# Kernel tuning notes

Hardware: AMD Instinct MI355X
Metric: run time of the kernel (lower is better)

Reference implementation:

```python
import jax, jax.numpy as jnp
import numpy as np

_EPS = 1e-8
_ALPHA = 160.0  # bilateral spatial sigma
_BETA = 3.0     # bilateral color sigma
_GAMMA = 3.0    # spatial-filter sigma
_NUM_ITERS = 5
_L = 21
_H = 96
_W = 96


def _spatial_features(h, w, sigma):
    # [h, w, 2] grid of (x, y)/sigma, matching torch _spatial_features
    x = jnp.arange(w, dtype=jnp.float32) / sigma
    y = jnp.arange(h, dtype=jnp.float32) / sigma
    xx = jnp.broadcast_to(x[None, :], (h, w))
    yy = jnp.broadcast_to(y[:, None], (h, w))
    return jnp.stack([xx, yy], axis=2)


def _gauss_kernel(f):
    # f: [N, d] -> exact Gaussian kernel exp(-0.5 ||f_i - f_j||^2), [N, N]
    sq = jnp.sum(f * f, axis=1)
    d2 = sq[:, None] + sq[None, :] - 2.0 * (f @ f.T)
    return jnp.exp(-0.5 * jnp.maximum(d2, 0.0))


def setup_inputs() -> dict:
    key = jax.random.key(0)
    k1, k2 = jax.random.split(key)
    image = jax.random.uniform(k1, (1, 3, _H, _W), dtype=jnp.float32)
    logits = jax.random.normal(k2, (1, _L, _H, _W), dtype=jnp.float32)
    eye = jnp.eye(_L, dtype=jnp.float32)
    return {
        "image": image,
        "logits": logits,
        "spatial_ker_weights": 3.0 * eye,
        "bilateral_ker_weights": 5.0 * eye,
        "compatibility_matrix": eye,
    }


def reference(image, logits, spatial_ker_weights, bilateral_ker_weights, compatibility_matrix):
    img = image[0]        # [3, h, w]
    unary = logits[0]     # [L, h, w]
    L, h, w = unary.shape
    N = h * w

    # Filter kernels (exact Gaussian filtering that the permutohedral lattice approximates)
    xy_s = _spatial_features(h, w, _GAMMA).reshape(N, 2)
    xy_b = _spatial_features(h, w, _ALPHA)
    rgb = (img / _BETA).transpose(1, 2, 0)  # [h, w, 3]
    feat_b = jnp.concatenate([xy_b, rgb], axis=2).reshape(N, 5)

    K_s = _gauss_kernel(xy_s)    # [N, N]
    K_b = _gauss_kernel(feat_b)  # [N, N]
    norm_s = 1.0 / (jnp.sum(K_s, axis=1) + _EPS)  # [N]
    norm_b = 1.0 / (jnp.sum(K_b, axis=1) + _EPS)

    unary_flat = unary.reshape(L, N)
    cur = unary_flat
    for _ in range(_NUM_ITERS):
        q = jax.nn.softmax(cur, axis=0)           # softmax over labels, [L, N]
        sp = spatial_ker_weights @ ((q @ K_s) * norm_s)    # K symmetric
        bl = bilateral_ker_weights @ ((q @ K_b) * norm_b)
        cur = compatibility_matrix @ (sp + bl) + unary_flat
    return cur.reshape(1, L, h, w)
```

## Files before the change

### kernel.cpp

```cpp
#include <hip/hip_runtime.h>

#define NPIX 9216
#define NL   21
#define WW   96
#define RAD  16
#define JS   16
#define NJC  576
#define NST  9
#define NIB  72
#define NBIL (NIB * JS)
#define NSPT 756
#define L2E  1.44269504088896340736f

typedef __bf16 bf16x8 __attribute__((ext_vector_type(8)));
typedef float  f32x16 __attribute__((ext_vector_type(16)));

__device__ __forceinline__ float fexp2(float x) { return __builtin_amdgcn_exp2f(x); }
__device__ __forceinline__ unsigned pkbf(float lo, float hi) {
    unsigned r;
    asm("v_cvt_pk_bf16_f32 %0, %1, %2" : "=v"(r) : "v"(lo), "v"(hi));
    return r;
}

__global__ __launch_bounds__(256) void featK(const float* __restrict__ img,
                                             __bf16* __restrict__ FiT8, __bf16* __restrict__ Fj8,
                                             float* __restrict__ norm_s, __bf16* __restrict__ QhT) {
    int i = blockIdx.x * 256 + threadIdx.x;
    if (i >= NPIX) return;
    int y = i / WW, x = i - y * WW;
    float f0 = (float)x * (1.0f / 160.0f);
    float f1 = (float)y * (1.0f / 160.0f);
    float f2 = img[0 * NPIX + i] * (1.0f / 3.0f);
    float f3 = img[1 * NPIX + i] * (1.0f / 3.0f);
    float f4 = img[2 * NPIX + i] * (1.0f / 3.0f);
    float st = 0.5f * (f0*f0 + f1*f1 + f2*f2 + f3*f3 + f4*f4) * L2E;
    __bf16* a = Fj8 + (size_t)i * 16;
    __bf16* b = FiT8 + (size_t)i * 16;
    a[0]=(__bf16)(f0*L2E); a[1]=(__bf16)(f1*L2E); a[2]=(__bf16)(f2*L2E);
    a[3]=(__bf16)(f3*L2E); a[4]=(__bf16)(f4*L2E); a[5]=(__bf16)st; a[6]=(__bf16)1.0f;
    b[0]=(__bf16)f0; b[1]=(__bf16)f1; b[2]=(__bf16)f2; b[3]=(__bf16)f3; b[4]=(__bf16)f4;
    b[5]=(__bf16)-1.0f; b[6]=(__bf16)(-st);
    #pragma unroll
    for (int k = 7; k < 16; k++) { a[k] = (__bf16)0.0f; b[k] = (__bf16)0.0f; }
    QhT[(size_t)21 * NPIX + i] = (__bf16)1.0f;
    #pragma unroll
    for (int l = 22; l < 32; l++) QhT[(size_t)l * NPIX + i] = (__bf16)0.0f;
    const float cs = (-0.5f / 9.0f) * L2E;
    float sx = 0.f, sy = 0.f;
    int xa = max(0, x - RAD), xb = min(WW - 1, x + RAD);
    int ya = max(0, y - RAD), yb = min(WW - 1, y + RAD);
    for (int t = xa; t <= xb; t++) { float dx = (float)(x - t); sx += fexp2(cs * dx * dx); }
    for (int t = ya; t <= yb; t++) { float dy = (float)(y - t); sy += fexp2(cs * dy * dy); }
    norm_s[i] = 1.0f / (sx * sy + 1e-8f);
}

__global__ __launch_bounds__(448) void matK(const float* __restrict__ Cm, const float* __restrict__ Wsm,
                                            const float* __restrict__ Wbm,
                                            float* __restrict__ Ms, float* __restrict__ Mb) {
    int t = threadIdx.x;
    if (t >= NL * NL) return;
    int l = t / NL, p = t - l * NL;
    float a = 0.f, b = 0.f;
    for (int m = 0; m < NL; m++) {
        float c = Cm[l * NL + m];
        a = fmaf(c, Wsm[m * NL + p], a);
        b = fmaf(c, Wbm[m * NL + p], b);
    }
    Ms[t] = a; Mb[t] = b;
}

__global__ __launch_bounds__(256) void smax0(const float* __restrict__ cur, __bf16* __restrict__ QhT) {
    int i = blockIdx.x * 256 + threadIdx.x;
    if (i >= NPIX) return;
    float v[NL]; float m = -1e30f;
    #pragma unroll
    for (int l = 0; l < NL; l++) { v[l] = cur[l * NPIX + i]; m = fmaxf(m, v[l]); }
    float s = 0.f;
    #pragma unroll
    for (int l = 0; l < NL; l++) { v[l] = fexp2((v[l] - m) * L2E); s += v[l]; }
    float inv = 1.0f / s;
    #pragma unroll
    for (int l = 0; l < NL; l++) QhT[(size_t)l * NPIX + i] = (__bf16)(v[l] * inv);
}

__global__ __launch_bounds__(256) void spatX(const __bf16* __restrict__ QhT, float* __restrict__ S1) {
    __shared__ float wt[33];
    int t = threadIdx.x;
    if (t < 33) { float d = (float)(t - RAD); wt[t] = fexp2((-0.5f / 9.0f) * L2E * d * d); }
    __syncthreads();
    int tid = blockIdx.x * 256 + t;
    int l = tid / NPIX, rem = tid - l * NPIX;
    int y = rem / WW, x1 = rem - y * WW;
    const __bf16* row = QhT + (size_t)l * NPIX + y * WW;
    float acc = 0.f;
    #pragma unroll
    for (int d = 0; d < 33; d++) {
        int x2 = x1 - RAD + d;
        if ((unsigned)x2 < WW) acc = fmaf(wt[d], (float)row[x2], acc);
    }
    S1[tid] = acc;
}

__global__ __launch_bounds__(256) void fusedYB(const __bf16* __restrict__ QhT,
                                               const __bf16* __restrict__ FiT8,
                                               const __bf16* __restrict__ Fj8,
                                               float* __restrict__ part,
                                               const float* __restrict__ S1,
                                               const float* __restrict__ norm_s,
                                               float* __restrict__ Sp) {
    __shared__ __bf16 sQ[2][32][72];
    __shared__ __bf16 sFj[2][64][24];
    __shared__ float wt[33];
    int t = threadIdx.x;

    if (blockIdx.x >= NBIL) {
        if (t < 33) { float d = (float)(t - RAD); wt[t] = fexp2((-0.5f / 9.0f) * L2E * d * d); }
        __syncthreads();
        int tid = (blockIdx.x - NBIL) * 256 + t;
        int l = tid / NPIX, rem = tid - l * NPIX;
        int y1 = rem / WW, x = rem - y1 * WW;
        const float* col = S1 + l * NPIX + x;
        float acc = 0.f;
        #pragma unroll
        for (int d = 0; d < 33; d++) {
            int y2 = y1 - RAD + d;
            if ((unsigned)y2 < WW) acc = fmaf(wt[d], col[y2 * WW], acc);
        }
        Sp[tid] = acc * norm_s[rem];
        return;
    }

    int lane = t & 63;
    int w = t >> 6;
    int n = lane & 31, kb = lane >> 5;
    int jc = blockIdx.x / NIB;
    int ib = blockIdx.x - jc * NIB;
    int ibase = ib * 128 + w * 32;

    bf16x8 b1 = *reinterpret_cast<const bf16x8*>(FiT8 + (size_t)(ibase + n) * 16 + kb * 8);

    int qr = t >> 3, qc = t & 7;
    int fr = t >> 1, fh = t & 1;
    int jbeg = jc * NJC;
    const __bf16* qsrc = QhT + (size_t)qr * NPIX + jbeg;
    const __bf16* fsrc = Fj8 + (size_t)jbeg * 16;

    float4 gq = *reinterpret_cast<const float4*>(qsrc + qc * 8);
    float4 gf;
    if (t < 128) gf = *reinterpret_cast<const float4*>(fsrc + fr * 16 + fh * 8);
    *reinterpret_cast<float4*>(&sQ[0][qr][qc * 8]) = gq;
    if (t < 128) *reinterpret_cast<float4*>(&sFj[0][fr][fh * 8]) = gf;

    f32x16 acc = {};
    const f32x16 z = {};
    int cur = 0;
    for (int s = 0; s < NST; s++) {
        __syncthreads();
        bool pf = (s + 1 < NST);
        if (pf) {
            int jo = (s + 1) * 64;
            gq = *reinterpret_cast<const float4*>(qsrc + jo + qc * 8);
            if (t < 128) gf = *reinterpret_cast<const float4*>(fsrc + (size_t)(jo + fr) * 16 + fh * 8);
        }
        #pragma unroll
        for (int t2 = 0; t2 < 2; t2++) {
            int t32 = t2 * 32;
            bf16x8 a1 = *reinterpret_cast<const bf16x8*>(&sFj[cur][t32 + n][kb * 8]);
            f32x16 d = __builtin_amdgcn_mfma_f32_32x32x16_bf16(a1, b1, z, 0, 0, 0);
            float e[16];
            #pragma unroll
            for (int q = 0; q < 16; q++) e[q] = fexp2(d[q]);
            #pragma unroll
            for (int h = 0; h < 2; h++) {
                unsigned w0 = pkbf(e[8*h+0], e[8*h+1]);
                unsigned w1 = pkbf(e[8*h+2], e[8*h+3]);
                unsigned w2 = pkbf(e[8*h+4], e[8*h+5]);
                unsigned w3 = pkbf(e[8*h+6], e[8*h+7]);
                asm volatile("v_permlane32_swap_b32 %0, %1" : "+v"(w0), "+v"(w2));
                asm volatile("v_permlane32_swap_b32 %0, %1" : "+v"(w1), "+v"(w3));
                union { int4 u4; bf16x8 h8; } bb;
                bb.u4 = make_int4(w0, w1, w2, w3);
                bf16x8 qa = *reinterpret_cast<const bf16x8*>(&sQ[cur][n][t32 + h * 16 + kb * 8]);
                acc = __builtin_amdgcn_mfma_f32_32x32x16_bf16(qa, bb.h8, acc, 0, 0, 0);
            }
        }
        if (pf) {
            int nx = cur ^ 1;
            *reinterpret_cast<float4*>(&sQ[nx][qr][qc * 8]) = gq;
            if (t < 128) *reinterpret_cast<float4*>(&sFj[nx][fr][fh * 8]) = gf;
        }
        cur ^= 1;
    }
    float* p = part + (size_t)jc * 22 * NPIX + ibase + n;
    #pragma unroll
    for (int q = 0; q < 16; q++) {
        int l = (q & 3) + 8 * (q >> 2) + 4 * kb;
        if (l < 22) p[(size_t)l * NPIX] = acc[q];
    }
}

__global__ __launch_bounds__(256) void combZ(const float* __restrict__ Sp, const float* __restrict__ part,
                                             const float* __restrict__ Ms, const float* __restrict__ Mb,
                                             const float* __restrict__ unary, float* __restrict__ outp,
                                             __bf16* __restrict__ QhT, int wq) {
    __shared__ float sMs[NL * NL], sMb[NL * NL];
    int t = threadIdx.x;
    for (int k = t; k < NL * NL; k += 256) { sMs[k] = Ms[k]; sMb[k] = Mb[k]; }
    __syncthreads();
    int i = blockIdx.x * 256 + t;
    if (i >= NPIX) return;
    float bl[22];
    #pragma unroll
    for (int l = 0; l < 22; l++) bl[l] = 0.0f;
    for (int jc = 0; jc < JS; jc++) {
        const float* p = part + (size_t)jc * 22 * NPIX + i;
        #pragma unroll
        for (int l = 0; l < 22; l++) bl[l] += p[(size_t)l * NPIX];
    }
    float inv = 1.0f / (bl[21] + 1e-8f);
    float sp[NL], v[NL];
    #pragma unroll
    for (int p = 0; p < NL; p++) { sp[p] = Sp[p * NPIX + i]; bl[p] *= inv; }
    #pragma unroll
    for (int l = 0; l < NL; l++) {
        float a = unary[l * NPIX + i];
        #pragma unroll
        for (int p = 0; p < NL; p++) {
            a = fmaf(sMs[l * NL + p], sp[p], a);
            a = fmaf(sMb[l * NL + p], bl[p], a);
        }
        outp[l * NPIX + i] = a;
        v[l] = a;
    }
    if (!wq) return;
    float m = -1e30f;
    #pragma unroll
    for (int l = 0; l < NL; l++) m = fmaxf(m, v[l]);
    float s = 0.f;
    #pragma unroll
    for (int l = 0; l < NL; l++) { v[l] = fexp2((v[l] - m) * L2E); s += v[l]; }
    float qi = 1.0f / s;
    #pragma unroll
    for (int l = 0; l < NL; l++) QhT[(size_t)l * NPIX + i] = (__bf16)(v[l] * qi);
}

extern "C" void kernel_launch(void* const* d_in, const int* in_sizes, int n_in,
                              void* d_out, int out_size, void* d_ws, size_t ws_size,
                              hipStream_t stream) {
    const float* img   = (const float*)d_in[0];
    const float* logit = (const float*)d_in[1];
    const float* Wsm   = (const float*)d_in[2];
    const float* Wbm   = (const float*)d_in[3];
    const float* Cm    = (const float*)d_in[4];
    float* out = (float*)d_out;
    float* ws  = (float*)d_ws;

    __bf16* FiT8  = (__bf16*)ws;
    __bf16* Fj8   = (__bf16*)(ws + 73728);
    float* S1     = ws + 147456;
    float* Sp     = ws + 340992;
    float* norm_s = ws + 534528;
    float* Ms     = ws + 543744;
    float* Mb     = ws + 544192;
    __bf16* QhT   = (__bf16*)(ws + 544640);
    float* part   = ws + 692096;

    featK<<<36, 256, 0, stream>>>(img, FiT8, Fj8, norm_s, QhT);
    matK<<<1, 448, 0, stream>>>(Cm, Wsm, Wbm, Ms, Mb);
    smax0<<<36, 256, 0, stream>>>(logit, QhT);
    for (int it = 0; it < 5; ++it) {
        spatX<<<756, 256, 0, stream>>>(QhT, S1);
        fusedYB<<<NBIL + NSPT, 256, 0, stream>>>(QhT, FiT8, Fj8, part, S1, norm_s, Sp);
        combZ<<<36, 256, 0, stream>>>(Sp, part, Ms, Mb, logit, out, QhT, it < 4 ? 1 : 0);
    }
}
```

Measured before the change: 226.8 us.

## Reduce bilateral split-K partials with atomics instead of a partial buffer

The bilateral MFMA kernel now accumulates its 16 j-chunk partial results directly into one accumulator buffer with float atomicAdd, instead of writing separate per-chunk slabs that combZ later sums. combZ reads the single reduced buffer, re-zeroes it for the next iteration, and runs with 64-thread blocks for more parallelism. This removes the write and re-read of 16x22xN partials, at the cost of atomic contention and non-deterministic summation order.

```diff
diff --git a/kernel.cpp b/kernel.cpp
--- a/kernel.cpp
+++ b/kernel.cpp
@@ -24,7 +24,8 @@
 
 __global__ __launch_bounds__(256) void featK(const float* __restrict__ img,
                                              __bf16* __restrict__ FiT8, __bf16* __restrict__ Fj8,
-                                             float* __restrict__ norm_s, __bf16* __restrict__ QhT) {
+                                             float* __restrict__ norm_s, __bf16* __restrict__ QhT,
+                                             float* __restrict__ Bl) {
     int i = blockIdx.x * 256 + threadIdx.x;
     if (i >= NPIX) return;
     int y = i / WW, x = i - y * WW;
@@ -45,6 +46,8 @@
     QhT[(size_t)21 * NPIX + i] = (__bf16)1.0f;
     #pragma unroll
     for (int l = 22; l < 32; l++) QhT[(size_t)l * NPIX + i] = (__bf16)0.0f;
+    #pragma unroll
+    for (int l = 0; l < 22; l++) Bl[(size_t)l * NPIX + i] = 0.0f;
     const float cs = (-0.5f / 9.0f) * L2E;
     float sx = 0.f, sy = 0.f;
     int xa = max(0, x - RAD), xb = min(WW - 1, x + RAD);
@@ -104,7 +107,7 @@
 __global__ __launch_bounds__(256) void fusedYB(const __bf16* __restrict__ QhT,
                                                const __bf16* __restrict__ FiT8,
                                                const __bf16* __restrict__ Fj8,
-                                               float* __restrict__ part,
+                                               float* __restrict__ Bl,
                                                const float* __restrict__ S1,
                                                const float* __restrict__ norm_s,
                                                float* __restrict__ Sp) {
@@ -191,36 +194,30 @@
         }
         cur ^= 1;
     }
-    float* p = part + (size_t)jc * 22 * NPIX + ibase + n;
+    int gi = ibase + n;
     #pragma unroll
     for (int q = 0; q < 16; q++) {
         int l = (q & 3) + 8 * (q >> 2) + 4 * kb;
-        if (l < 22) p[(size_t)l * NPIX] = acc[q];
-    }
-}
-
-__global__ __launch_bounds__(256) void combZ(const float* __restrict__ Sp, const float* __restrict__ part,
-                                             const float* __restrict__ Ms, const float* __restrict__ Mb,
-                                             const float* __restrict__ unary, float* __restrict__ outp,
-                                             __bf16* __restrict__ QhT, int wq) {
+        if (l < 22) atomicAdd(&Bl[(size_t)l * NPIX + gi], acc[q]);
+    }
+}
+
+__global__ __launch_bounds__(64) void combZ(const float* __restrict__ Sp, float* __restrict__ Bl,
+                                            const float* __restrict__ Ms, const float* __restrict__ Mb,
+                                            const float* __restrict__ unary, float* __restrict__ outp,
+                                            __bf16* __restrict__ QhT, int wq) {
     __shared__ float sMs[NL * NL], sMb[NL * NL];
     int t = threadIdx.x;
-    for (int k = t; k < NL * NL; k += 256) { sMs[k] = Ms[k]; sMb[k] = Mb[k]; }
+    for (int k = t; k < NL * NL; k += 64) { sMs[k] = Ms[k]; sMb[k] = Mb[k]; }
     __syncthreads();
-    int i = blockIdx.x * 256 + t;
+    int i = blockIdx.x * 64 + t;
     if (i >= NPIX) return;
-    float bl[22];
-    #pragma unroll
-    for (int l = 0; l < 22; l++) bl[l] = 0.0f;
-    for (int jc = 0; jc < JS; jc++) {
-        const float* p = part + (size_t)jc * 22 * NPIX + i;
-        #pragma unroll
-        for (int l = 0; l < 22; l++) bl[l] += p[(size_t)l * NPIX];
-    }
-    float inv = 1.0f / (bl[21] + 1e-8f);
-    float sp[NL], v[NL];
-    #pragma unroll
-    for (int p = 0; p < NL; p++) { sp[p] = Sp[p * NPIX + i]; bl[p] *= inv; }
+    float inv = 1.0f / (Bl[(size_t)21 * NPIX + i] + 1e-8f);
+    float sp[NL], bl[NL], v[NL];
+    #pragma unroll
+    for (int p = 0; p < NL; p++) { sp[p] = Sp[p * NPIX + i]; bl[p] = Bl[p * NPIX + i] * inv; }
+    #pragma unroll
+    for (int l = 0; l < 22; l++) Bl[(size_t)l * NPIX + i] = 0.0f;
     #pragma unroll
     for (int l = 0; l < NL; l++) {
         float a = unary[l * NPIX + i];
@@ -259,18 +256,18 @@
     __bf16* Fj8   = (__bf16*)(ws + 73728);
     float* S1     = ws + 147456;
     float* Sp     = ws + 340992;
-    float* norm_s = ws + 534528;
-    float* Ms     = ws + 543744;
-    float* Mb     = ws + 544192;
-    __bf16* QhT   = (__bf16*)(ws + 544640);
-    float* part   = ws + 692096;
-
-    featK<<<36, 256, 0, stream>>>(img, FiT8, Fj8, norm_s, QhT);
+    float* Bl     = ws + 534528;
+    float* norm_s = ws + 737280;
+    float* Ms     = ws + 746496;
+    float* Mb     = ws + 746944;
+    __bf16* QhT   = (__bf16*)(ws + 747392);
+
+    featK<<<36, 256, 0, stream>>>(img, FiT8, Fj8, norm_s, QhT, Bl);
     matK<<<1, 448, 0, stream>>>(Cm, Wsm, Wbm, Ms, Mb);
     smax0<<<36, 256, 0, stream>>>(logit, QhT);
     for (int it = 0; it < 5; ++it) {
         spatX<<<756, 256, 0, stream>>>(QhT, S1);
-        fusedYB<<<NBIL + NSPT, 256, 0, stream>>>(QhT, FiT8, Fj8, part, S1, norm_s, Sp);
-        combZ<<<36, 256, 0, stream>>>(Sp, part, Ms, Mb, logit, out, QhT, it < 4 ? 1 : 0);
-    }
-}
+        fusedYB<<<NBIL + NSPT, 256, 0, stream>>>(QhT, FiT8, Fj8, Bl, S1, norm_s, Sp);
+        combZ<<<144, 64, 0, stream>>>(Sp, Bl, Ms, Mb, logit, out, QhT, it < 4 ? 1 : 0);
+    }
+}
```

Result: faster. 218.1 us (-3.8%).
